# Kernel optimization log

Measured on AMD Instinct MI355X. Metric: run time of the kernel, lower is better.

Reference implementation:

```python
import jax, jax.numpy as jnp
import numpy as np

DIM = 512
PART = 6
EXP = 4
EPS = 1e-5

def setup_inputs() -> dict:
    key = jax.random.key(0)
    ks = jax.random.split(key, 6)
    B, N = 1024, 162
    x = jax.random.normal(ks[0], (B, N, DIM), dtype=jnp.float32)
    part_tokens = jax.random.normal(ks[1], (PART, DIM), dtype=jnp.float32) * (2.0 / DIM) ** 0.5
    ln_g = jnp.ones((DIM,), dtype=jnp.float32)
    ln_b = jnp.zeros((DIM,), dtype=jnp.float32)
    W1 = jax.random.normal(ks[2], (DIM, EXP * DIM), dtype=jnp.float32) * (1.0 / DIM) ** 0.5
    b1 = jnp.zeros((EXP * DIM,), dtype=jnp.float32)
    W2 = jax.random.normal(ks[3], (EXP * DIM, DIM), dtype=jnp.float32) * (1.0 / (EXP * DIM)) ** 0.5
    b2 = jnp.zeros((DIM,), dtype=jnp.float32)
    return {"x": x, "part_tokens": part_tokens, "ln_g": ln_g, "ln_b": ln_b,
            "W1": W1, "b1": b1, "W2": W2, "b2": b2}

def reference(x, part_tokens, ln_g, ln_b, W1, b1, W2, b2):
    scaling = DIM ** 0.5
    # attention: [P,d] x [B,N,d] -> [B,P,N]
    attn = jnp.einsum('pd,bnd->bpn', part_tokens, x)
    attn = jax.nn.softmax(attn, axis=-1)
    # [B,P,N] x [B,N,d] -> [B,P,d], then post-scale (as in source)
    y = jnp.einsum('bpn,bnd->bpd', attn, x) / scaling
    # FeedForwardBlock: LayerNorm -> Linear -> GELU -> (dropout=identity) -> Linear
    mu = jnp.mean(y, axis=-1, keepdims=True)
    var = jnp.mean(jnp.square(y - mu), axis=-1, keepdims=True)
    h = (y - mu) * jax.lax.rsqrt(var + EPS) * ln_g + ln_b
    h = jax.nn.gelu(h @ W1 + b1, approximate=False)
    return h @ W2 + b2
```

## Files before the change

### kernel.cpp

```cpp
#include <hip/hip_runtime.h>
#include <hip/hip_bf16.h>

constexpr int   DIMC  = 512;
constexpr int   PARTC = 6;
constexpr int   NTOK  = 162;
constexpr float SCALING = 22.62741699796952f;
constexpr float LNEPS   = 1e-5f;

typedef __attribute__((ext_vector_type(8))) short bf16x8;
typedef __attribute__((ext_vector_type(4))) float f32x4;

__device__ __forceinline__ unsigned int pack_bf16(float a, float b) {
  __hip_bfloat16 h0 = __float2bfloat16(a);
  __hip_bfloat16 h1 = __float2bfloat16(b);
  return (unsigned int)*(unsigned short*)&h0 |
         ((unsigned int)*(unsigned short*)&h1 << 16);
}
__device__ __forceinline__ float bf_lo(unsigned int u) {
  return __uint_as_float(u << 16);
}
__device__ __forceinline__ float bf_hi(unsigned int u) {
  return __uint_as_float(u & 0xffff0000u);
}

__global__ __launch_bounds__(256) void transpose_f32_bf16(
    const float* __restrict__ in, __hip_bfloat16* __restrict__ outp, int R, int C)
{
  __shared__ float tile[32][33];
  const int tx = threadIdx.x, ty = threadIdx.y;
  const int bx = blockIdx.x, by = blockIdx.y;
  const int c = bx * 32 + tx;
#pragma unroll
  for (int i = 0; i < 32; i += 8) {
    int r = by * 32 + ty + i;
    tile[ty + i][tx] = in[(size_t)r * C + c];
  }
  __syncthreads();
#pragma unroll
  for (int i = 0; i < 32; i += 8) {
    outp[(size_t)(bx * 32 + ty + i) * R + by * 32 + tx] =
        __float2bfloat16(tile[tx][ty + i]);
  }
}

__global__ __launch_bounds__(256, 4) void attn_ln_k(
    const float* __restrict__ x,
    const float* __restrict__ pt,
    const float* __restrict__ g,
    const float* __restrict__ bta,
    __hip_bfloat16* __restrict__ outp)
{
  const int b = blockIdx.x;
  const int tid = threadIdx.x;
  const int w = tid >> 6;
  const int lane = tid & 63;
  const float* __restrict__ xb = x + (size_t)b * (NTOK * DIMC);

  __shared__ __align__(16) float ulds[2][PARTC][DIMC];
  __shared__ float s_lw[4][PARTC];
  __shared__ float s_red[4][2 * PARTC];

  unsigned int ptp[PARTC][4];
#pragma unroll
  for (int p = 0; p < PARTC; ++p) {
    const float* pr = pt + p * DIMC + 8 * lane;
    float4 a = *(const float4*)pr;
    float4 c = *(const float4*)(pr + 4);
    ptp[p][0] = pack_bf16(a.x, a.y);
    ptp[p][1] = pack_bf16(a.z, a.w);
    ptp[p][2] = pack_bf16(c.x, c.y);
    ptp[p][3] = pack_bf16(c.z, c.w);
  }

  float u[PARTC][8];
  float l[PARTC];
#pragma unroll
  for (int p = 0; p < PARTC; ++p) {
    l[p] = 0.f;
#pragma unroll
    for (int j = 0; j < 8; ++j) u[p][j] = 0.f;
  }

  for (int n = w; n < NTOK; n += 4) {
    const float* xr = xb + (size_t)n * DIMC + 8 * lane;
    f32x4 xa = __builtin_nontemporal_load((const f32x4*)xr);
    f32x4 xc = __builtin_nontemporal_load((const f32x4*)(xr + 4));

    float acc[PARTC];
#pragma unroll
    for (int p = 0; p < PARTC; ++p) {
      acc[p] = xa[0] * bf_lo(ptp[p][0]) + xa[1] * bf_hi(ptp[p][0])
             + xa[2] * bf_lo(ptp[p][1]) + xa[3] * bf_hi(ptp[p][1])
             + xc[0] * bf_lo(ptp[p][2]) + xc[1] * bf_hi(ptp[p][2])
             + xc[2] * bf_lo(ptp[p][3]) + xc[3] * bf_hi(ptp[p][3]);
    }
#pragma unroll
    for (int off = 32; off > 0; off >>= 1) {
#pragma unroll
      for (int p = 0; p < PARTC; ++p) acc[p] += __shfl_xor(acc[p], off);
    }
#pragma unroll
    for (int p = 0; p < PARTC; ++p) {
      const float we = __expf(acc[p]);
      l[p] += we;
      u[p][0] += we * xa[0]; u[p][1] += we * xa[1];
      u[p][2] += we * xa[2]; u[p][3] += we * xa[3];
      u[p][4] += we * xc[0]; u[p][5] += we * xc[1];
      u[p][6] += we * xc[2]; u[p][7] += we * xc[3];
    }
  }

  if (w >= 2) {
#pragma unroll
    for (int p = 0; p < PARTC; ++p) {
      *(float4*)&ulds[w - 2][p][8 * lane]     = make_float4(u[p][0], u[p][1], u[p][2], u[p][3]);
      *(float4*)&ulds[w - 2][p][8 * lane + 4] = make_float4(u[p][4], u[p][5], u[p][6], u[p][7]);
    }
    if (lane == 0) {
#pragma unroll
      for (int p = 0; p < PARTC; ++p) s_lw[w][p] = l[p];
    }
  }
  __syncthreads();
  if (w < 2) {
#pragma unroll
    for (int p = 0; p < PARTC; ++p) {
      float4 a = *(const float4*)&ulds[w][p][8 * lane];
      float4 c = *(const float4*)&ulds[w][p][8 * lane + 4];
      a.x += u[p][0]; a.y += u[p][1]; a.z += u[p][2]; a.w += u[p][3];
      c.x += u[p][4]; c.y += u[p][5]; c.z += u[p][6]; c.w += u[p][7];
      *(float4*)&ulds[w][p][8 * lane]     = a;
      *(float4*)&ulds[w][p][8 * lane + 4] = c;
    }
    if (lane == 0) {
#pragma unroll
      for (int p = 0; p < PARTC; ++p) s_lw[w][p] = l[p];
    }
  }
  __syncthreads();

  float lt[PARTC];
#pragma unroll
  for (int p = 0; p < PARTC; ++p)
    lt[p] = s_lw[0][p] + s_lw[1][p] + s_lw[2][p] + s_lw[3][p];

  float y0[PARTC], y1[PARTC], s1[PARTC], s2[PARTC];
#pragma unroll
  for (int p = 0; p < PARTC; ++p) {
    const float uu0 = ulds[0][p][2 * tid]     + ulds[1][p][2 * tid];
    const float uu1 = ulds[0][p][2 * tid + 1] + ulds[1][p][2 * tid + 1];
    const float inv = 1.f / (lt[p] * SCALING);
    y0[p] = uu0 * inv;
    y1[p] = uu1 * inv;
    s1[p] = y0[p] + y1[p];
    s2[p] = y0[p] * y0[p] + y1[p] * y1[p];
  }
#pragma unroll
  for (int off = 32; off > 0; off >>= 1) {
#pragma unroll
    for (int p = 0; p < PARTC; ++p) {
      s1[p] += __shfl_xor(s1[p], off);
      s2[p] += __shfl_xor(s2[p], off);
    }
  }
  if (lane == 0) {
#pragma unroll
    for (int p = 0; p < PARTC; ++p) {
      s_red[w][p] = s1[p];
      s_red[w][PARTC + p] = s2[p];
    }
  }
  __syncthreads();

  const float ga0 = g[2 * tid], ga1 = g[2 * tid + 1];
  const float bb0 = bta[2 * tid], bb1 = bta[2 * tid + 1];
  __hip_bfloat16* orow = outp + (size_t)b * PARTC * DIMC;
#pragma unroll
  for (int p = 0; p < PARTC; ++p) {
    float S = s_red[0][p] + s_red[1][p] + s_red[2][p] + s_red[3][p];
    float Q = s_red[0][PARTC + p] + s_red[1][PARTC + p] + s_red[2][PARTC + p] + s_red[3][PARTC + p];
    float mu = S * (1.f / 512.f);
    float var = Q * (1.f / 512.f) - mu * mu;
    float r = rsqrtf(var + LNEPS);
    __hip_bfloat162 hv;
    hv.x = __float2bfloat16((y0[p] - mu) * r * ga0 + bb0);
    hv.y = __float2bfloat16((y1[p] - mu) * r * ga1 + bb1);
    *(__hip_bfloat162*)(orow + p * DIMC + 2 * tid) = hv;
  }
}

template <int BM, int BN, bool GELU>
__global__ __launch_bounds__(256) void gemm_bt(
    const __hip_bfloat16* __restrict__ A,
    const __hip_bfloat16* __restrict__ Bt,
    const float* __restrict__ bias,
    void* __restrict__ Cv,
    int M, int N, int K)
{
  constexpr int BK = 64;
  constexpr int LDT = BK + 16;
  __shared__ __align__(16) unsigned short Al[BM][LDT];
  __shared__ __align__(16) unsigned short Bl[BN][LDT];

  const int tid = threadIdx.x;
  const int w = tid >> 6, lane = tid & 63;
  const int wr = w >> 1, wc = w & 1;
  const int tm = blockIdx.y * BM, tn = blockIdx.x * BN;
  constexpr int FM = BM / 32, FN = BN / 32;

  f32x4 acc[FM][FN];
#pragma unroll
  for (int m = 0; m < FM; ++m)
#pragma unroll
    for (int n = 0; n < FN; ++n) acc[m][n] = (f32x4){0.f, 0.f, 0.f, 0.f};

  const int srow = tid >> 3;
  const int scol = (tid & 7) * 8;

  for (int k0 = 0; k0 < K; k0 += BK) {
    __syncthreads();
#pragma unroll
    for (int r = 0; r < BM / 32; ++r) {
      int row = r * 32 + srow;
      *(int4*)(&Al[row][scol]) =
          *(const int4*)(A + (size_t)(tm + row) * K + k0 + scol);
    }
#pragma unroll
    for (int r = 0; r < BN / 32; ++r) {
      int row = r * 32 + srow;
      *(int4*)(&Bl[row][scol]) =
          *(const int4*)(Bt + (size_t)(tn + row) * K + k0 + scol);
    }
    __syncthreads();

#pragma unroll
    for (int kk = 0; kk < 2; ++kk) {
      const int ko = kk * 32 + (lane >> 4) * 8;
      bf16x8 af[FM], bfr[FN];
#pragma unroll
      for (int m = 0; m < FM; ++m)
        af[m] = *(const bf16x8*)(&Al[wr * (BM / 2) + m * 16 + (lane & 15)][ko]);
#pragma unroll
      for (int n = 0; n < FN; ++n)
        bfr[n] = *(const bf16x8*)(&Bl[wc * (BN / 2) + n * 16 + (lane & 15)][ko]);
#pragma unroll
      for (int m = 0; m < FM; ++m)
#pragma unroll
        for (int n = 0; n < FN; ++n)
          acc[m][n] = __builtin_amdgcn_mfma_f32_16x16x32_bf16(
              af[m], bfr[n], acc[m][n], 0, 0, 0);
    }
  }

  const int cl = lane & 15, rg = (lane >> 4) * 4;
#pragma unroll
  for (int m = 0; m < FM; ++m) {
#pragma unroll
    for (int n = 0; n < FN; ++n) {
      int col = tn + wc * (BN / 2) + n * 16 + cl;
      float bv = bias[col];
#pragma unroll
      for (int r = 0; r < 4; ++r) {
        int row = tm + wr * (BM / 2) + m * 16 + rg + r;
        float v = acc[m][n][r] + bv;
        if (GELU) {
          v = 0.5f * v * (1.f + erff(v * 0.7071067811865476f));
          ((__hip_bfloat16*)Cv)[(size_t)row * N + col] = __float2bfloat16(v);
        } else {
          ((float*)Cv)[(size_t)row * N + col] = v;
        }
      }
    }
  }
}

extern "C" void kernel_launch(void* const* d_in, const int* in_sizes, int n_in,
                              void* d_out, int out_size, void* d_ws, size_t ws_size,
                              hipStream_t stream)
{
  const float* x   = (const float*)d_in[0];
  const float* pt  = (const float*)d_in[1];
  const float* g   = (const float*)d_in[2];
  const float* bta = (const float*)d_in[3];
  const float* W1  = (const float*)d_in[4];
  const float* b1  = (const float*)d_in[5];
  const float* W2  = (const float*)d_in[6];
  const float* b2  = (const float*)d_in[7];
  float* outp = (float*)d_out;

  char* ws = (char*)d_ws;
  __hip_bfloat16* W1T = (__hip_bfloat16*)(ws);
  __hip_bfloat16* W2T = (__hip_bfloat16*)(ws + 2097152);
  __hip_bfloat16* LNO = (__hip_bfloat16*)(ws + 4194304);
  __hip_bfloat16* H   = (__hip_bfloat16*)(ws + 10485760);

  transpose_f32_bf16<<<dim3(2048 / 32, 512 / 32), dim3(32, 8), 0, stream>>>(W1, W1T, 512, 2048);
  transpose_f32_bf16<<<dim3(512 / 32, 2048 / 32), dim3(32, 8), 0, stream>>>(W2, W2T, 2048, 512);

  attn_ln_k<<<1024, 256, 0, stream>>>(x, pt, g, bta, LNO);

  gemm_bt<128, 128, true><<<dim3(2048 / 128, 6144 / 128), 256, 0, stream>>>(
      LNO, W1T, b1, (void*)H, 6144, 2048, 512);

  gemm_bt<128, 64, false><<<dim3(512 / 64, 6144 / 128), 256, 0, stream>>>(
      H, W2T, b2, (void*)outp, 6144, 512, 2048);
}
```

Baseline: 174.1 us.

## Split attention parts across wave pairs with 512-thread blocks

The attention+LayerNorm kernel now launches 512 threads per batch row. Each pair of waves shares a token stride, and each wave of the pair handles 3 of the 6 part tokens, which halves per-thread accumulators and register pressure. Each wave still loads the x rows itself, so every x row is read twice (once per wave of the pair), likely absorbed by cache. The LayerNorm epilogue is remapped to one element per thread with an 8-wave reduction.

```diff
diff --git a/kernel.cpp b/kernel.cpp
--- a/kernel.cpp
+++ b/kernel.cpp
@@ -43,7 +43,7 @@
   }
 }
 
-__global__ __launch_bounds__(256, 4) void attn_ln_k(
+__global__ __launch_bounds__(512, 4) void attn_ln_k(
     const float* __restrict__ x,
     const float* __restrict__ pt,
     const float* __restrict__ g,
@@ -54,16 +54,19 @@
   const int tid = threadIdx.x;
   const int w = tid >> 6;
   const int lane = tid & 63;
+  const int q = w >> 1;
+  const int ph = w & 1;
+  const int pbase = 3 * ph;
   const float* __restrict__ xb = x + (size_t)b * (NTOK * DIMC);
 
   __shared__ __align__(16) float ulds[2][PARTC][DIMC];
-  __shared__ float s_lw[4][PARTC];
-  __shared__ float s_red[4][2 * PARTC];
-
-  unsigned int ptp[PARTC][4];
-#pragma unroll
-  for (int p = 0; p < PARTC; ++p) {
-    const float* pr = pt + p * DIMC + 8 * lane;
+  __shared__ float s_lw[8][3];
+  __shared__ float s_red[8][2 * PARTC];
+
+  unsigned int ptp[3][4];
+#pragma unroll
+  for (int p = 0; p < 3; ++p) {
+    const float* pr = pt + (pbase + p) * DIMC + 8 * lane;
     float4 a = *(const float4*)pr;
     float4 c = *(const float4*)(pr + 4);
     ptp[p][0] = pack_bf16(a.x, a.y);
@@ -72,23 +75,23 @@
     ptp[p][3] = pack_bf16(c.z, c.w);
   }
 
-  float u[PARTC][8];
-  float l[PARTC];
-#pragma unroll
-  for (int p = 0; p < PARTC; ++p) {
+  float u[3][8];
+  float l[3];
+#pragma unroll
+  for (int p = 0; p < 3; ++p) {
     l[p] = 0.f;
 #pragma unroll
     for (int j = 0; j < 8; ++j) u[p][j] = 0.f;
   }
 
-  for (int n = w; n < NTOK; n += 4) {
+  for (int n = q; n < NTOK; n += 4) {
     const float* xr = xb + (size_t)n * DIMC + 8 * lane;
     f32x4 xa = __builtin_nontemporal_load((const f32x4*)xr);
     f32x4 xc = __builtin_nontemporal_load((const f32x4*)(xr + 4));
 
-    float acc[PARTC];
-#pragma unroll
-    for (int p = 0; p < PARTC; ++p) {
+    float acc[3];
+#pragma unroll
+    for (int p = 0; p < 3; ++p) {
       acc[p] = xa[0] * bf_lo(ptp[p][0]) + xa[1] * bf_hi(ptp[p][0])
              + xa[2] * bf_lo(ptp[p][1]) + xa[3] * bf_hi(ptp[p][1])
              + xc[0] * bf_lo(ptp[p][2]) + xc[1] * bf_hi(ptp[p][2])
@@ -97,10 +100,10 @@
 #pragma unroll
     for (int off = 32; off > 0; off >>= 1) {
 #pragma unroll
-      for (int p = 0; p < PARTC; ++p) acc[p] += __shfl_xor(acc[p], off);
-    }
-#pragma unroll
-    for (int p = 0; p < PARTC; ++p) {
+      for (int p = 0; p < 3; ++p) acc[p] += __shfl_xor(acc[p], off);
+    }
+#pragma unroll
+    for (int p = 0; p < 3; ++p) {
       const float we = __expf(acc[p]);
       l[p] += we;
       u[p][0] += we * xa[0]; u[p][1] += we * xa[1];
@@ -110,50 +113,48 @@
     }
   }
 
-  if (w >= 2) {
-#pragma unroll
-    for (int p = 0; p < PARTC; ++p) {
-      *(float4*)&ulds[w - 2][p][8 * lane]     = make_float4(u[p][0], u[p][1], u[p][2], u[p][3]);
-      *(float4*)&ulds[w - 2][p][8 * lane + 4] = make_float4(u[p][4], u[p][5], u[p][6], u[p][7]);
-    }
-    if (lane == 0) {
-#pragma unroll
-      for (int p = 0; p < PARTC; ++p) s_lw[w][p] = l[p];
+  if (lane == 0) {
+#pragma unroll
+    for (int p = 0; p < 3; ++p) s_lw[w][p] = l[p];
+  }
+  if (w >= 4) {
+    const int slot = (w - 4) >> 1;
+#pragma unroll
+    for (int p = 0; p < 3; ++p) {
+      *(float4*)&ulds[slot][pbase + p][8 * lane]     = make_float4(u[p][0], u[p][1], u[p][2], u[p][3]);
+      *(float4*)&ulds[slot][pbase + p][8 * lane + 4] = make_float4(u[p][4], u[p][5], u[p][6], u[p][7]);
     }
   }
   __syncthreads();
-  if (w < 2) {
-#pragma unroll
-    for (int p = 0; p < PARTC; ++p) {
-      float4 a = *(const float4*)&ulds[w][p][8 * lane];
-      float4 c = *(const float4*)&ulds[w][p][8 * lane + 4];
+  if (w < 4) {
+    const int slot = w >> 1;
+#pragma unroll
+    for (int p = 0; p < 3; ++p) {
+      float4 a = *(const float4*)&ulds[slot][pbase + p][8 * lane];
+      float4 c = *(const float4*)&ulds[slot][pbase + p][8 * lane + 4];
       a.x += u[p][0]; a.y += u[p][1]; a.z += u[p][2]; a.w += u[p][3];
       c.x += u[p][4]; c.y += u[p][5]; c.z += u[p][6]; c.w += u[p][7];
-      *(float4*)&ulds[w][p][8 * lane]     = a;
-      *(float4*)&ulds[w][p][8 * lane + 4] = c;
-    }
-    if (lane == 0) {
-#pragma unroll
-      for (int p = 0; p < PARTC; ++p) s_lw[w][p] = l[p];
+      *(float4*)&ulds[slot][pbase + p][8 * lane]     = a;
+      *(float4*)&ulds[slot][pbase + p][8 * lane + 4] = c;
     }
   }
   __syncthreads();
 
   float lt[PARTC];
 #pragma unroll
-  for (int p = 0; p < PARTC; ++p)
-    lt[p] = s_lw[0][p] + s_lw[1][p] + s_lw[2][p] + s_lw[3][p];
-
-  float y0[PARTC], y1[PARTC], s1[PARTC], s2[PARTC];
-#pragma unroll
   for (int p = 0; p < PARTC; ++p) {
-    const float uu0 = ulds[0][p][2 * tid]     + ulds[1][p][2 * tid];
-    const float uu1 = ulds[0][p][2 * tid + 1] + ulds[1][p][2 * tid + 1];
+    const int phv = p / 3, lp = p - 3 * phv;
+    lt[p] = s_lw[phv][lp] + s_lw[phv + 2][lp] + s_lw[phv + 4][lp] + s_lw[phv + 6][lp];
+  }
+
+  float y0[PARTC], s1[PARTC], s2[PARTC];
+#pragma unroll
+  for (int p = 0; p < PARTC; ++p) {
+    const float uu = ulds[0][p][tid] + ulds[1][p][tid];
     const float inv = 1.f / (lt[p] * SCALING);
-    y0[p] = uu0 * inv;
-    y1[p] = uu1 * inv;
-    s1[p] = y0[p] + y1[p];
-    s2[p] = y0[p] * y0[p] + y1[p] * y1[p];
+    y0[p] = uu * inv;
+    s1[p] = y0[p];
+    s2[p] = y0[p] * y0[p];
   }
 #pragma unroll
   for (int off = 32; off > 0; off >>= 1) {
@@ -172,20 +173,20 @@
   }
   __syncthreads();
 
-  const float ga0 = g[2 * tid], ga1 = g[2 * tid + 1];
-  const float bb0 = bta[2 * tid], bb1 = bta[2 * tid + 1];
+  const float ga = g[tid], ba = bta[tid];
   __hip_bfloat16* orow = outp + (size_t)b * PARTC * DIMC;
 #pragma unroll
   for (int p = 0; p < PARTC; ++p) {
-    float S = s_red[0][p] + s_red[1][p] + s_red[2][p] + s_red[3][p];
-    float Q = s_red[0][PARTC + p] + s_red[1][PARTC + p] + s_red[2][PARTC + p] + s_red[3][PARTC + p];
+    float S = 0.f, Q = 0.f;
+#pragma unroll
+    for (int ww = 0; ww < 8; ++ww) {
+      S += s_red[ww][p];
+      Q += s_red[ww][PARTC + p];
+    }
     float mu = S * (1.f / 512.f);
     float var = Q * (1.f / 512.f) - mu * mu;
     float r = rsqrtf(var + LNEPS);
-    __hip_bfloat162 hv;
-    hv.x = __float2bfloat16((y0[p] - mu) * r * ga0 + bb0);
-    hv.y = __float2bfloat16((y1[p] - mu) * r * ga1 + bb1);
-    *(__hip_bfloat162*)(orow + p * DIMC + 2 * tid) = hv;
+    orow[p * DIMC + tid] = __float2bfloat16((y0[p] - mu) * r * ga + ba);
   }
 }
 
@@ -297,7 +298,7 @@
   transpose_f32_bf16<<<dim3(2048 / 32, 512 / 32), dim3(32, 8), 0, stream>>>(W1, W1T, 512, 2048);
   transpose_f32_bf16<<<dim3(512 / 32, 2048 / 32), dim3(32, 8), 0, stream>>>(W2, W2T, 2048, 512);
 
-  attn_ln_k<<<1024, 256, 0, stream>>>(x, pt, g, bta, LNO);
+  attn_ln_k<<<1024, 512, 0, stream>>>(x, pt, g, bta, LNO);
 
   gemm_bt<128, 128, true><<<dim3(2048 / 128, 6144 / 128), 256, 0, stream>>>(
       LNO, W1T, b1, (void*)H, 6144, 2048, 512);
```

After: 196.0 us. 12.6% more time.
